# Kernel optimization log

Measured on AMD Instinct MI355X. Metric: run time of the kernel, lower is better.

Reference implementation:

```python
import jax, jax.numpy as jnp
import numpy as np

B, S, D_MODEL = 1, 2048, 2048
N_HEADS, N_KV_HEADS, D_HEAD = 16, 4, 128
ROTARY_DIM, ROTARY_BASE = 128, 10000.0
ATTN_SCALE = float(np.sqrt(D_HEAD))
REPEAT = N_HEADS // N_KV_HEADS


def _sin_cos_rotary(n_ctx, rotary_dim, base):
    # TransformerLens calculate_sin_cos_rotary, rotary_adjacent_pairs=False:
    # freq repeated as 'd -> (2 d)'
    pos = jnp.arange(n_ctx, dtype=jnp.float32)
    dim = jnp.arange(rotary_dim // 2, dtype=jnp.float32)
    freq = base ** (dim / (rotary_dim / 2))
    freq = jnp.concatenate([freq, freq])  # (2 d)
    angles = pos[:, None] / freq[None, :]  # [n_ctx, rotary_dim]
    return jnp.sin(angles), jnp.cos(angles)


def _rotate_every_two_half(x):
    # rotate_half for non-adjacent pairs: [-x2, x1]
    d = x.shape[-1]
    return jnp.concatenate([-x[..., d // 2:], x[..., : d // 2]], axis=-1)


def _apply_rotary(x, sin, cos):
    # x: [batch, pos, head, d_head]; sin/cos: [n_ctx, rotary_dim]
    p = x.shape[1]
    s = sin[:p][:, None, :]  # [pos, 1, rotary_dim]
    c = cos[:p][:, None, :]
    x_rot = x[..., :ROTARY_DIM]
    x_pass = x[..., ROTARY_DIM:]
    x_rotated = x_rot * c + _rotate_every_two_half(x_rot) * s
    return jnp.concatenate([x_rotated, x_pass], axis=-1)


def setup_inputs() -> dict:
    key = jax.random.key(0)
    ks = jax.random.split(key, 10)
    init = 1.0 / np.sqrt(D_MODEL)
    return {
        "query_input": jax.random.normal(ks[0], (B, S, D_MODEL), jnp.float32),
        "key_input": jax.random.normal(ks[1], (B, S, D_MODEL), jnp.float32),
        "value_input": jax.random.normal(ks[2], (B, S, D_MODEL), jnp.float32),
        "W_Q": jax.random.normal(ks[3], (N_HEADS, D_MODEL, D_HEAD), jnp.float32) * init,
        "b_Q": jnp.zeros((N_HEADS, D_HEAD), jnp.float32),
        "W_K": jax.random.normal(ks[4], (N_KV_HEADS, D_MODEL, D_HEAD), jnp.float32) * init,
        "b_K": jnp.zeros((N_KV_HEADS, D_HEAD), jnp.float32),
        "W_V": jax.random.normal(ks[5], (N_KV_HEADS, D_MODEL, D_HEAD), jnp.float32) * init,
        "b_V": jnp.zeros((N_KV_HEADS, D_HEAD), jnp.float32),
        "W_O": jax.random.normal(ks[6], (N_HEADS, D_HEAD, D_MODEL), jnp.float32) * init,
        "b_O": jnp.zeros((D_MODEL,), jnp.float32),
    }


def reference(query_input, key_input, value_input, W_Q, b_Q, W_K, b_K, W_V, b_V, W_O, b_O):
    sin, cos = _sin_cos_rotary(S, ROTARY_DIM, ROTARY_BASE)

    # Projections
    q = jnp.einsum("bpd,hdk->bphk", query_input, W_Q) + b_Q   # [B,S,H,dh]
    k = jnp.einsum("bpd,hdk->bphk", key_input, W_K) + b_K     # [B,S,Hkv,dh]
    v = jnp.einsum("bpd,hdk->bphk", value_input, W_V) + b_V   # [B,S,Hkv,dh]

    # Rotary on q and k (before KV head expansion)
    q = _apply_rotary(q, sin, cos)
    k = _apply_rotary(k, sin, cos)

    # GQA expansion via repeat_interleave on head dim
    k = jnp.repeat(k, REPEAT, axis=2)  # [B,S,H,dh]
    v = jnp.repeat(v, REPEAT, axis=2)

    # Attention scores, causal mask, softmax
    scores = jnp.einsum("bqhd,bkhd->bhqk", q, k) / ATTN_SCALE  # [B,H,S,S]
    causal = jnp.tril(jnp.ones((S, S), dtype=bool))
    scores = jnp.where(causal, scores, jnp.finfo(scores.dtype).min)
    pattern = jax.nn.softmax(scores, axis=-1)

    # Weighted values and output projection
    z = jnp.einsum("bhqk,bkhd->bqhd", pattern, v)              # [B,S,H,dh]
    out = jnp.einsum("bqhd,hdm->bqm", z, W_O) + b_O            # [B,S,D]
    return out
```

## Files before the change

### kernel.cpp

```cpp
#include <hip/hip_runtime.h>
#include <hip/hip_bf16.h>
#include <stdint.h>
#include <math.h>

typedef __bf16 bf16_t;
typedef __attribute__((ext_vector_type(8))) __bf16 bf16x8;
typedef __attribute__((ext_vector_type(4))) __bf16 bf16x4;
typedef __attribute__((ext_vector_type(4))) float f32x4;
typedef __attribute__((ext_vector_type(16))) float f32x16;
typedef unsigned int uint2v __attribute__((ext_vector_type(2)));

static constexpr int S = 2048;
static constexpr int DM = 2048;
static constexpr int NH = 16;
static constexpr int NKV = 4;
static constexpr int DH = 128;

#define MFMA16(a, b, c) __builtin_amdgcn_mfma_f32_16x16x32_bf16((a), (b), (c), 0, 0, 0)
#define MFMA32(a, b, c) __builtin_amdgcn_mfma_f32_32x32x16_bf16((a), (b), (c), 0, 0, 0)

__device__ __forceinline__ void gload_lds16(const void* g, void* l) {
  __builtin_amdgcn_global_load_lds((__attribute__((address_space(1))) void*)(g),
                                   (__attribute__((address_space(3))) void*)(l), 16, 0, 0);
}

template <int N>
__device__ __forceinline__ void wait_vmcnt() {
  asm volatile("s_waitcnt vmcnt(%0)" :: "n"(N) : "memory");
}
__device__ __forceinline__ void wait_lgkm0() {
  asm volatile("s_waitcnt lgkmcnt(0)" ::: "memory");
}

__device__ __forceinline__ unsigned cvtpk(float lo, float hi) {
  unsigned r;
  asm("v_cvt_pk_bf16_f32 %0, %1, %2" : "=v"(r) : "v"(lo), "v"(hi));
  return r;
}
__device__ __forceinline__ void plswap2(unsigned& a, unsigned& b) {
  uint2v r = __builtin_amdgcn_permlane32_swap(a, b, false, false);
  a = r[0]; b = r[1];
}
__device__ __forceinline__ float swapred_max(float x) {
  uint2v r = __builtin_amdgcn_permlane32_swap(__float_as_uint(x), __float_as_uint(x), false, false);
  return fmaxf(__uint_as_float(r[0]), __uint_as_float(r[1]));
}
__device__ __forceinline__ float swapred_sum(float x) {
  uint2v r = __builtin_amdgcn_permlane32_swap(__float_as_uint(x), __float_as_uint(x), false, false);
  return __uint_as_float(r[0]) + __uint_as_float(r[1]);
}
__device__ __forceinline__ bf16x8 packfrag(float a0, float a1, float a2, float a3,
                                           float a4, float a5, float a6, float a7) {
  unsigned w0 = cvtpk(a0, a1), w1 = cvtpk(a2, a3);
  unsigned w2 = cvtpk(a4, a5), w3 = cvtpk(a6, a7);
  plswap2(w0, w2); plswap2(w1, w3);
  union { unsigned u[4]; bf16x8 v; } u;
  u.u[0] = w0; u.u[1] = w1; u.u[2] = w2; u.u[3] = w3;
  return u.v;
}

__device__ const unsigned char attn_map[61] = {
  120,121,122,123,124,125,126, 112,113,114,115,116,117, 104,105,106,107,108,109,
  96,97,98,99,100,101, 88,89,90,91,92, 80,81,82,83,84, 72,73,74,75, 64,65,66,67,
  56,57,58,59, 48,49,50, 40,41,42, 32,33, 24,25, 16,17, 8, 0};
__device__ const unsigned char sbase[16] = {0,0,0,2,4,6,9,12,16,20,24,29,34,40,46,52};

__global__ __launch_bounds__(256)
void prep_k(const float* __restrict__ Xq, const float* __restrict__ Xk,
            const float* __restrict__ Xv, const float* __restrict__ WQ,
            const float* __restrict__ WK, const float* __restrict__ WV,
            const float* __restrict__ WO, float2* __restrict__ tab,
            bf16_t* __restrict__ xq, bf16_t* __restrict__ xk, bf16_t* __restrict__ xv,
            bf16_t* __restrict__ wqT, bf16_t* __restrict__ wkT, bf16_t* __restrict__ wvT,
            bf16_t* __restrict__ woT) {
  __shared__ float tile[32][33];
  const int b = blockIdx.x, t = threadIdx.x;
  if (b < 512) {
    int idx = b * 256 + t;
    int p = idx >> 6, j = idx & 63;
    double inv = exp2(-(double)j * 13.287712379549449 / 64.0);
    double ang = (double)p * inv;
    tab[idx] = make_float2((float)sin(ang), (float)cos(ang));
  } else if (b < 12800) {
    int i = ((b - 512) * 256 + t) * 4;
    const float* in; bf16_t* out; int off;
    if (i < 4194304) { in = Xq; out = xq; off = i; }
    else if (i < 8388608) { in = Xk; out = xk; off = i - 4194304; }
    else { in = Xv; out = xv; off = i - 8388608; }
    f32x4 v = *(const f32x4*)(in + off);
    bf16x4 o;
    o[0] = (bf16_t)v[0]; o[1] = (bf16_t)v[1]; o[2] = (bf16_t)v[2]; o[3] = (bf16_t)v[3];
    *(bf16x4*)(out + off) = o;
  } else if (b < 16896) {
    int b2 = b - 12800;
    int bx = b2 & 3, by = (b2 >> 2) & 63, bz = b2 >> 8;
    int c0 = bx * 32, r0 = by * 32;
    int tx = t & 31, ty = t >> 5;
    const float* src = WQ + (size_t)bz * 2048 * 128;
    #pragma unroll
    for (int j = 0; j < 32; j += 8)
      tile[ty + j][tx] = src[(size_t)(r0 + ty + j) * 128 + c0 + tx];
    __syncthreads();
    #pragma unroll
    for (int j = 0; j < 32; j += 8)
      wqT[(size_t)(bz * 128 + c0 + ty + j) * 2048 + r0 + tx] = (bf16_t)tile[tx][ty + j];
  } else if (b < 18944) {
    int b2 = b - 16896;
    int bx = b2 & 3, by = (b2 >> 2) & 63, bz = b2 >> 8;
    int g = bz & 3;
    const float* in = (bz < 4) ? WK : WV;
    bf16_t* out = (bz < 4) ? wkT : wvT;
    int c0 = bx * 32, r0 = by * 32;
    int tx = t & 31, ty = t >> 5;
    const float* src = in + (size_t)g * 2048 * 128;
    #pragma unroll
    for (int j = 0; j < 32; j += 8)
      tile[ty + j][tx] = src[(size_t)(r0 + ty + j) * 128 + c0 + tx];
    __syncthreads();
    #pragma unroll
    for (int j = 0; j < 32; j += 8)
      out[(size_t)(g * 128 + c0 + ty + j) * 2048 + r0 + tx] = (bf16_t)tile[tx][ty + j];
  } else {
    int b2 = b - 18944;
    int bx = b2 & 63, by = (b2 >> 6) & 3, bz = b2 >> 8;
    int c0 = bx * 32, r0 = by * 32;
    int tx = t & 31, ty = t >> 5;
    const float* src = WO + (size_t)bz * 128 * 2048;
    #pragma unroll
    for (int j = 0; j < 32; j += 8)
      tile[ty + j][tx] = src[(size_t)(r0 + ty + j) * 2048 + c0 + tx];
    __syncthreads();
    #pragma unroll
    for (int j = 0; j < 32; j += 8)
      woT[(size_t)(c0 + ty + j) * 2048 + bz * 128 + r0 + tx] = (bf16_t)tile[tx][ty + j];
  }
}

__global__ void rope_qk_k(bf16_t* __restrict__ Qb, bf16_t* __restrict__ Kb,
                          const float2* __restrict__ tab, float qscale) {
  int tid = blockIdx.x * 256 + threadIdx.x;
  int row = tid >> 4;
  int i = (tid & 15) * 4;
  bf16_t* base; float scale;
  if (row < NH * S) { base = Qb + (size_t)row * DH; scale = qscale; }
  else { base = Kb + (size_t)(row - NH * S) * DH; scale = 1.0f; }
  int p = row & (S - 1);
  bf16x4 lo = *(bf16x4*)(base + i);
  bf16x4 hi = *(bf16x4*)(base + i + 64);
  float4 t0 = *(const float4*)(tab + p * 64 + i);
  float4 t1 = *(const float4*)(tab + p * 64 + i + 2);
  float sv[4] = {t0.x, t0.z, t1.x, t1.z};
  float cv[4] = {t0.y, t0.w, t1.y, t1.w};
  bf16x4 nlo, nhi;
  #pragma unroll
  for (int j = 0; j < 4; ++j) {
    float a = (float)lo[j], b = (float)hi[j];
    nlo[j] = (bf16_t)((a * cv[j] - b * sv[j]) * scale);
    nhi[j] = (bf16_t)((b * cv[j] + a * sv[j]) * scale);
  }
  *(bf16x4*)(base + i) = nlo;
  *(bf16x4*)(base + i + 64) = nhi;
}

__global__ __launch_bounds__(256)
void proj_gemm_k(const bf16_t* __restrict__ xq, const bf16_t* __restrict__ xk,
                 const bf16_t* __restrict__ xv, const bf16_t* __restrict__ wqT,
                 const bf16_t* __restrict__ wkT, const bf16_t* __restrict__ wvT,
                 const float* __restrict__ bQ, const float* __restrict__ bK,
                 const float* __restrict__ bV, bf16_t* __restrict__ Qb,
                 bf16_t* __restrict__ Kb, bf16_t* __restrict__ Vt) {
  const int b = blockIdx.x;
  const int xcd = b & 7, idx = b >> 3;
  const int nb = (xcd & 3) * 12 + idx % 12;
  const int m0 = ((xcd >> 2) * 8 + idx / 12) * 128;
  const bf16_t* A; const bf16_t* B; const float* bias; bf16_t* dst; int ncol0;
  bool vmode = false;
  if (nb < 32)      { A = xq; B = wqT; bias = bQ; dst = Qb; ncol0 = nb * 64; }
  else if (nb < 40) { A = xk; B = wkT; bias = bK; dst = Kb; ncol0 = (nb - 32) * 64; }
  else              { A = xv; B = wvT; bias = bV; dst = Vt; ncol0 = (nb - 40) * 64; vmode = true; }
  const int K = 2048;
  const int t = threadIdx.x;
  const int lane = t & 63, w = t >> 6;
  const int l15 = lane & 15, lg = lane >> 4;
  const int wr = (w >> 1) * 64, wc = (w & 1) * 32;

  __shared__ bf16_t lA[2][128 * 64];
  __shared__ bf16_t lB[2][64 * 64];

  f32x4 acc[4][2] = {};
  const int srow = t >> 3;
  const int sslot = t & 7;

  auto stage = [&](int buf, int kt) {
    #pragma unroll
    for (int i = 0; i < 4; ++i) {
      int row = i * 32 + srow;
      int ss = sslot ^ (row & 7);
      gload_lds16(A + (size_t)(m0 + row) * K + kt * 64 + ss * 8,
                  (void*)(&lA[buf][0] + i * 2048 + t * 8));
    }
    #pragma unroll
    for (int i = 0; i < 2; ++i) {
      int row = i * 32 + srow;
      int ss = sslot ^ (row & 7);
      gload_lds16(B + (size_t)(ncol0 + row) * K + kt * 64 + ss * 8,
                  (void*)(&lB[buf][0] + i * 2048 + t * 8));
    }
  };

  const int nk = K >> 6;
  stage(0, 0);
  for (int kt = 0; kt < nk; ++kt) {
    const int cur = kt & 1;
    if (kt + 1 < nk) {
      stage(cur ^ 1, kt + 1);
      wait_vmcnt<6>();
    } else {
      wait_vmcnt<0>();
    }
    __builtin_amdgcn_s_barrier();
    #pragma unroll
    for (int kk = 0; kk < 2; ++kk) {
      bf16x8 af[4], bfv[2];
      #pragma unroll
      for (int f = 0; f < 4; ++f) {
        int row = wr + f * 16 + l15;
        int slot = kk * 4 + lg;
        af[f] = *(const bf16x8*)(&lA[cur][0] + row * 64 + ((slot ^ (row & 7)) * 8));
      }
      #pragma unroll
      for (int f = 0; f < 2; ++f) {
        int row = wc + f * 16 + l15;
        int slot = kk * 4 + lg;
        bfv[f] = *(const bf16x8*)(&lB[cur][0] + row * 64 + ((slot ^ (row & 7)) * 8));
      }
      #pragma unroll
      for (int fm = 0; fm < 4; ++fm)
        #pragma unroll
        for (int fn = 0; fn < 2; ++fn)
          acc[fm][fn] = MFMA16(af[fm], bfv[fn], acc[fm][fn]);
    }
    wait_lgkm0();
    __builtin_amdgcn_s_barrier();
  }

  #pragma unroll
  for (int fm = 0; fm < 4; ++fm) {
    int rowb = m0 + wr + fm * 16 + lg * 4;
    #pragma unroll
    for (int fn = 0; fn < 2; ++fn) {
      int col = ncol0 + wc + fn * 16 + l15;
      float bb = bias[col];
      if (vmode) {
        bf16x4 pk;
        #pragma unroll
        for (int r = 0; r < 4; ++r) pk[r] = (bf16_t)(acc[fm][fn][r] + bb);
        *(bf16x4*)(dst + (size_t)col * S + rowb) = pk;
      } else {
        #pragma unroll
        for (int r = 0; r < 4; ++r) {
          float v = acc[fm][fn][r] + bb;
          dst[((size_t)(col >> 7) * S + (rowb + r)) * DH + (col & 127)] = (bf16_t)v;
        }
      }
    }
  }
}

__global__ __launch_bounds__(256)
void gemm_o_k(const bf16_t* __restrict__ A, const bf16_t* __restrict__ B,
              const float* __restrict__ bias, float* __restrict__ Cout) {
  const int b = blockIdx.x;
  const int xcd = b & 7, idx = b >> 3;
  const int ncol0 = ((xcd & 3) * 8 + (idx & 7)) * 64;
  const int m0 = (((xcd >> 2) * 8) + (idx >> 3)) * 128;
  const int K = 2048;
  const int t = threadIdx.x;
  const int lane = t & 63, w = t >> 6;
  const int l15 = lane & 15, lg = lane >> 4;
  const int wr = (w >> 1) * 64, wc = (w & 1) * 32;

  __shared__ bf16_t lA[2][128 * 64];
  __shared__ bf16_t lB[2][64 * 64];

  f32x4 acc[4][2] = {};
  const int srow = t >> 3;
  const int sslot = t & 7;

  auto stage = [&](int buf, int kt) {
    #pragma unroll
    for (int i = 0; i < 4; ++i) {
      int row = i * 32 + srow;
      int ss = sslot ^ (row & 7);
      gload_lds16(A + (size_t)(m0 + row) * K + kt * 64 + ss * 8,
                  (void*)(&lA[buf][0] + i * 2048 + t * 8));
    }
    #pragma unroll
    for (int i = 0; i < 2; ++i) {
      int row = i * 32 + srow;
      int ss = sslot ^ (row & 7);
      gload_lds16(B + (size_t)(ncol0 + row) * K + kt * 64 + ss * 8,
                  (void*)(&lB[buf][0] + i * 2048 + t * 8));
    }
  };

  const int nk = K >> 6;
  stage(0, 0);
  for (int kt = 0; kt < nk; ++kt) {
    const int cur = kt & 1;
    if (kt + 1 < nk) {
      stage(cur ^ 1, kt + 1);
      wait_vmcnt<6>();
    } else {
      wait_vmcnt<0>();
    }
    __builtin_amdgcn_s_barrier();
    #pragma unroll
    for (int kk = 0; kk < 2; ++kk) {
      bf16x8 af[4], bfv[2];
      #pragma unroll
      for (int f = 0; f < 4; ++f) {
        int row = wr + f * 16 + l15;
        int slot = kk * 4 + lg;
        af[f] = *(const bf16x8*)(&lA[cur][0] + row * 64 + ((slot ^ (row & 7)) * 8));
      }
      #pragma unroll
      for (int f = 0; f < 2; ++f) {
        int row = wc + f * 16 + l15;
        int slot = kk * 4 + lg;
        bfv[f] = *(const bf16x8*)(&lB[cur][0] + row * 64 + ((slot ^ (row & 7)) * 8));
      }
      #pragma unroll
      for (int fm = 0; fm < 4; ++fm)
        #pragma unroll
        for (int fn = 0; fn < 2; ++fn)
          acc[fm][fn] = MFMA16(af[fm], bfv[fn], acc[fm][fn]);
    }
    wait_lgkm0();
    __builtin_amdgcn_s_barrier();
  }

  #pragma unroll
  for (int fm = 0; fm < 4; ++fm) {
    int rowb = m0 + wr + fm * 16 + lg * 4;
    #pragma unroll
    for (int fn = 0; fn < 2; ++fn) {
      int col = ncol0 + wc + fn * 16 + l15;
      float bb = bias[col];
      #pragma unroll
      for (int r = 0; r < 4; ++r)
        Cout[(size_t)(rowb + r) * DM + col] = acc[fm][fn][r] + bb;
    }
  }
}

__global__ __launch_bounds__(256, 2)
void attn_k(const bf16_t* __restrict__ Q, const bf16_t* __restrict__ K,
            const bf16_t* __restrict__ Vt, bf16_t* __restrict__ Z,
            bf16_t* __restrict__ Opart, float* __restrict__ mpart,
            float* __restrict__ lpart) {
  const int bid = blockIdx.x;
  const int h = bid & 15;
  const int g = bid >> 4;
  const int code = attn_map[g];
  const int qb = code >> 3, ci = code & 7;
  const bool split = qb >= 2;
  const int kt0 = 5 * ci;
  const int kteA = 5 * ci + 4, kteB = 2 * qb + 1;
  const int ktend = kteA < kteB ? kteA : kteB;
  const int q0 = qb * 128;
  const int hkv = h >> 2;
  const int t = threadIdx.x;
  const int lane = t & 63, w = t >> 6;
  const int l31 = lane & 31, hi = lane >> 5;
  const int qrow = q0 + w * 32 + l31;

  __shared__ bf16_t lK[2][64 * 128];
  __shared__ bf16_t lV[2][128 * 64];

  bf16x8 qf[8];
  #pragma unroll
  for (int j = 0; j < 8; ++j)
    qf[j] = *(const bf16x8*)(Q + ((size_t)h * S + qrow) * DH + j * 16 + hi * 8);

  auto stageKV = [&](int buf, int kt) {
    #pragma unroll
    for (int i = 0; i < 4; ++i) {
      int row = i * 16 + (t >> 4);
      int ss = (t & 15) ^ (row & 15);
      gload_lds16(K + ((size_t)hkv * S + kt * 64 + row) * DH + ss * 8,
                  (void*)(&lK[buf][0] + i * 2048 + t * 8));
    }
    #pragma unroll
    for (int i = 0; i < 4; ++i) {
      int row = i * 32 + (t >> 3);
      int ss = (t & 7) ^ (row & 7);
      gload_lds16(Vt + ((size_t)hkv * DH + row) * S + kt * 64 + ss * 8,
                  (void*)(&lV[buf][0] + i * 2048 + t * 8));
    }
  };

  f32x16 oacc0 = {}, oacc1 = {}, oacc2 = {}, oacc3 = {};
  float m_run = -3.0e3f, l_run = 0.f;

  stageKV(0, kt0);
  for (int kt = kt0; kt <= ktend; ++kt) {
    const int cur = (kt - kt0) & 1;
    if (kt < ktend) {
      stageKV(cur ^ 1, kt + 1);
      wait_vmcnt<8>();
    } else {
      wait_vmcnt<0>();
    }
    __builtin_amdgcn_s_barrier();

    f32x16 s0 = {}, s1 = {};
    __builtin_amdgcn_s_setprio(1);
    #pragma unroll
    for (int j = 0; j < 8; ++j) {
      int sIdx = j * 2 + hi;
      int r0 = l31;
      bf16x8 k0 = *(const bf16x8*)(&lK[cur][0] + r0 * 128 + ((sIdx ^ (r0 & 15)) * 8));
      s0 = MFMA32(k0, qf[j], s0);
      int r1 = 32 + l31;
      bf16x8 k1 = *(const bf16x8*)(&lK[cur][0] + r1 * 128 + ((sIdx ^ (r1 & 15)) * 8));
      s1 = MFMA32(k1, qf[j], s1);
    }
    __builtin_amdgcn_s_setprio(0);

    if (kt >= 2 * qb) {
      #pragma unroll
      for (int r = 0; r < 16; ++r) {
        int krow = kt * 64 + (r & 3) + 8 * (r >> 2) + 4 * hi;
        if (krow > qrow) s0[r] = -1e30f;
        if (krow + 32 > qrow) s1[r] = -1e30f;
      }
    }

    float mxa = s0[0], mxb = s0[1], mxc = s0[2], mxd = s0[3];
    #pragma unroll
    for (int r = 4; r < 16; r += 4) {
      mxa = fmaxf(mxa, s0[r]); mxb = fmaxf(mxb, s0[r + 1]);
      mxc = fmaxf(mxc, s0[r + 2]); mxd = fmaxf(mxd, s0[r + 3]);
    }
    #pragma unroll
    for (int r = 0; r < 16; r += 4) {
      mxa = fmaxf(mxa, s1[r]); mxb = fmaxf(mxb, s1[r + 1]);
      mxc = fmaxf(mxc, s1[r + 2]); mxd = fmaxf(mxd, s1[r + 3]);
    }
    float mfull = swapred_max(fmaxf(fmaxf(mxa, mxb), fmaxf(mxc, mxd)));

    float m_new, alpha;
    bool nore = __all(mfull - m_run <= 8.0f);
    if (nore) { m_new = m_run; alpha = 1.0f; }
    else { m_new = fmaxf(m_run, mfull); alpha = exp2f(m_run - m_new); }

    float psa = 0.f, psb = 0.f, psc = 0.f, psd = 0.f;
    #pragma unroll
    for (int r = 0; r < 16; r += 4) {
      s0[r] = exp2f(s0[r] - m_new); psa += s0[r];
      s0[r + 1] = exp2f(s0[r + 1] - m_new); psb += s0[r + 1];
      s0[r + 2] = exp2f(s0[r + 2] - m_new); psc += s0[r + 2];
      s0[r + 3] = exp2f(s0[r + 3] - m_new); psd += s0[r + 3];
    }
    #pragma unroll
    for (int r = 0; r < 16; r += 4) {
      s1[r] = exp2f(s1[r] - m_new); psa += s1[r];
      s1[r + 1] = exp2f(s1[r + 1] - m_new); psb += s1[r + 1];
      s1[r + 2] = exp2f(s1[r + 2] - m_new); psc += s1[r + 2];
      s1[r + 3] = exp2f(s1[r + 3] - m_new); psd += s1[r + 3];
    }
    float lt = swapred_sum((psa + psb) + (psc + psd));
    l_run = l_run * alpha + lt;
    m_run = m_new;

    if (!nore) {
      #pragma unroll
      for (int r = 0; r < 16; ++r) {
        int qs = (r & 3) + 8 * (r >> 2) + 4 * hi;
        float ar = __shfl(alpha, qs);
        oacc0[r] *= ar; oacc1[r] *= ar; oacc2[r] *= ar; oacc3[r] *= ar;
      }
    }

    bf16x8 pa[4];
    pa[0] = packfrag(s0[0], s0[1], s0[2], s0[3], s0[4], s0[5], s0[6], s0[7]);
    pa[1] = packfrag(s0[8], s0[9], s0[10], s0[11], s0[12], s0[13], s0[14], s0[15]);
    pa[2] = packfrag(s1[0], s1[1], s1[2], s1[3], s1[4], s1[5], s1[6], s1[7]);
    pa[3] = packfrag(s1[8], s1[9], s1[10], s1[11], s1[12], s1[13], s1[14], s1[15]);

    __builtin_amdgcn_s_setprio(1);
#define PVBLK(OA, db) { \
    int dr = (db) * 32 + l31; \
    _Pragma("unroll") \
    for (int ks = 0; ks < 4; ++ks) { \
      int sIdx = ks * 2 + hi; \
      bf16x8 vf = *(const bf16x8*)(&lV[cur][0] + dr * 64 + ((sIdx ^ (dr & 7)) * 8)); \
      OA = MFMA32(pa[ks], vf, OA); \
    } }
    PVBLK(oacc0, 0)
    PVBLK(oacc1, 1)
    PVBLK(oacc2, 2)
    PVBLK(oacc3, 3)
#undef PVBLK
    __builtin_amdgcn_s_setprio(0);
    wait_lgkm0();
    __builtin_amdgcn_s_barrier();
  }

  if (!split) {
    float linv = 1.0f / l_run;
    #pragma unroll
    for (int r = 0; r < 16; ++r) {
      int qs = (r & 3) + 8 * (r >> 2) + 4 * hi;
      float lv = __shfl(linv, qs);
      int qg = q0 + w * 32 + qs;
      bf16_t* zp = Z + (size_t)qg * DM + h * DH + l31;
      zp[0]  = (bf16_t)(oacc0[r] * lv);
      zp[32] = (bf16_t)(oacc1[r] * lv);
      zp[64] = (bf16_t)(oacc2[r] * lv);
      zp[96] = (bf16_t)(oacc3[r] * lv);
    }
  } else {
    const int slot = h * 59 + sbase[qb] + ci;
    bf16_t* Op = Opart + (size_t)slot * 16384;
    #pragma unroll
    for (int r = 0; r < 16; ++r) {
      int qs = (r & 3) + 8 * (r >> 2) + 4 * hi;
      bf16_t* op = Op + (w * 32 + qs) * 128 + l31;
      op[0]  = (bf16_t)oacc0[r];
      op[32] = (bf16_t)oacc1[r];
      op[64] = (bf16_t)oacc2[r];
      op[96] = (bf16_t)oacc3[r];
    }
    if (lane < 32) {
      mpart[slot * 128 + w * 32 + l31] = m_run;
      lpart[slot * 128 + w * 32 + l31] = l_run;
    }
  }
}

__global__ void combine_k(const bf16_t* __restrict__ Opart, const float* __restrict__ mpart,
                          const float* __restrict__ lpart, bf16_t* __restrict__ Z) {
  int tid = blockIdx.x * 256 + threadIdx.x;
  int d4 = tid & 31;
  int q = (tid >> 5) & 127;
  int u = tid >> 12;
  int h = u / 14;
  int qb = 2 + (u - h * 14);
  int nc = (2 * qb + 6) / 5;
  int slot0 = h * 59 + sbase[qb];
  float M = -3.0e3f;
  for (int c = 0; c < nc; ++c) M = fmaxf(M, mpart[(slot0 + c) * 128 + q]);
  float L = 0.f;
  float o0 = 0.f, o1 = 0.f, o2 = 0.f, o3 = 0.f;
  for (int c = 0; c < nc; ++c) {
    float a = exp2f(mpart[(slot0 + c) * 128 + q] - M);
    L += a * lpart[(slot0 + c) * 128 + q];
    bf16x4 ov = *(const bf16x4*)(Opart + (size_t)(slot0 + c) * 16384 + q * 128 + d4 * 4);
    o0 += a * (float)ov[0]; o1 += a * (float)ov[1];
    o2 += a * (float)ov[2]; o3 += a * (float)ov[3];
  }
  float inv = 1.0f / L;
  bf16x4 zv;
  zv[0] = (bf16_t)(o0 * inv); zv[1] = (bf16_t)(o1 * inv);
  zv[2] = (bf16_t)(o2 * inv); zv[3] = (bf16_t)(o3 * inv);
  int qg = qb * 128 + q;
  *(bf16x4*)(Z + (size_t)qg * DM + h * DH + d4 * 4) = zv;
}

extern "C" void kernel_launch(void* const* d_in, const int* in_sizes, int n_in,
                              void* d_out, int out_size, void* d_ws, size_t ws_size,
                              hipStream_t stream) {
  (void)in_sizes; (void)n_in; (void)out_size; (void)ws_size;
  const float* Xq = (const float*)d_in[0];
  const float* Xk = (const float*)d_in[1];
  const float* Xv = (const float*)d_in[2];
  const float* WQ = (const float*)d_in[3];
  const float* bQ = (const float*)d_in[4];
  const float* WK = (const float*)d_in[5];
  const float* bK = (const float*)d_in[6];
  const float* WV = (const float*)d_in[7];
  const float* bV = (const float*)d_in[8];
  const float* WO = (const float*)d_in[9];
  const float* bO = (const float*)d_in[10];

  char* w = (char*)d_ws;
  float2* tab = (float2*)w;
  bf16_t* xq  = (bf16_t*)(w + (1 << 20));
  bf16_t* xk  = xq + 4194304;
  bf16_t* xv  = xk + 4194304;
  bf16_t* wqT = xv + 4194304;
  bf16_t* wkT = wqT + 4194304;
  bf16_t* wvT = wkT + 1048576;
  bf16_t* woT = wvT + 1048576;
  bf16_t* Qb  = woT + 4194304;
  bf16_t* Kb  = Qb + 4194304;
  bf16_t* Vtb = Kb + 1048576;
  bf16_t* Zb  = Vtb + 1048576;
  bf16_t* Opart = xq;
  float* mpart = (float*)tab;
  float* lpart = mpart + 944 * 128;

  prep_k<<<dim3(23040), dim3(256), 0, stream>>>(Xq, Xk, Xv, WQ, WK, WV, WO, tab,
                                                xq, xk, xv, wqT, wkT, wvT, woT);

  proj_gemm_k<<<dim3(768), dim3(256), 0, stream>>>(xq, xk, xv, wqT, wkT, wvT,
                                                   bQ, bK, bV, Qb, Kb, Vtb);

  const float qscale = 1.4426950408889634f / sqrtf(128.0f);
  rope_qk_k<<<dim3(2560), dim3(256), 0, stream>>>(Qb, Kb, tab, qscale);

  attn_k<<<dim3(976), dim3(256), 0, stream>>>(Qb, Kb, Vtb, Zb, Opart, mpart, lpart);
  combine_k<<<dim3(3584), dim3(256), 0, stream>>>(Opart, mpart, lpart, Zb);

  gemm_o_k<<<dim3(512), dim3(256), 0, stream>>>(Zb, woT, bO, (float*)d_out);
}
```

Baseline: 142.8 us.

## Use 128-key attention tiles with single-buffered K/V and resplit work chunks

```diff
diff --git a/kernel.cpp b/kernel.cpp
--- a/kernel.cpp
+++ b/kernel.cpp
@@ -59,11 +59,11 @@
   return u.v;
 }
 
-__device__ const unsigned char attn_map[61] = {
-  120,121,122,123,124,125,126, 112,113,114,115,116,117, 104,105,106,107,108,109,
-  96,97,98,99,100,101, 88,89,90,91,92, 80,81,82,83,84, 72,73,74,75, 64,65,66,67,
-  56,57,58,59, 48,49,50, 40,41,42, 32,33, 24,25, 16,17, 8, 0};
-__device__ const unsigned char sbase[16] = {0,0,0,2,4,6,9,12,16,20,24,29,34,40,46,52};
+__device__ const unsigned char attn_map[51] = {
+  120,121,122,123,124, 112,113,114,115,116, 104,105,106,107, 96,97,98,99,
+  88,89,90,91, 80,81,82, 72,73,74, 64,65,66, 56,57, 48,49, 40,41, 32, 24, 16,
+  108, 83, 58, 33, 8, 125, 100, 75, 50, 25, 0};
+__device__ const unsigned char sbase[16] = {0,0,0,0,2,4,6,9,12,15,19,23,27,32,37,42};
 
 __global__ __launch_bounds__(256)
 void prep_k(const float* __restrict__ Xq, const float* __restrict__ Xk,
@@ -364,10 +364,9 @@
   const int g = bid >> 4;
   const int code = attn_map[g];
   const int qb = code >> 3, ci = code & 7;
-  const bool split = qb >= 2;
-  const int kt0 = 5 * ci;
-  const int kteA = 5 * ci + 4, kteB = 2 * qb + 1;
-  const int ktend = kteA < kteB ? kteA : kteB;
+  const bool split = qb >= 3;
+  const int it0 = 3 * ci;
+  const int itend = (3 * ci + 2 < qb) ? (3 * ci + 2) : qb;
   const int q0 = qb * 128;
   const int hkv = h >> 2;
   const int t = threadIdx.x;
@@ -375,78 +374,75 @@
   const int l31 = lane & 31, hi = lane >> 5;
   const int qrow = q0 + w * 32 + l31;
 
-  __shared__ bf16_t lK[2][64 * 128];
-  __shared__ bf16_t lV[2][128 * 64];
+  __shared__ bf16_t lK[128 * 128];
+  __shared__ bf16_t lV[128 * 128];
 
   bf16x8 qf[8];
   #pragma unroll
   for (int j = 0; j < 8; ++j)
     qf[j] = *(const bf16x8*)(Q + ((size_t)h * S + qrow) * DH + j * 16 + hi * 8);
 
-  auto stageKV = [&](int buf, int kt) {
-    #pragma unroll
-    for (int i = 0; i < 4; ++i) {
+  auto stageKV = [&](int it) {
+    #pragma unroll
+    for (int i = 0; i < 8; ++i) {
       int row = i * 16 + (t >> 4);
       int ss = (t & 15) ^ (row & 15);
-      gload_lds16(K + ((size_t)hkv * S + kt * 64 + row) * DH + ss * 8,
-                  (void*)(&lK[buf][0] + i * 2048 + t * 8));
-    }
-    #pragma unroll
-    for (int i = 0; i < 4; ++i) {
-      int row = i * 32 + (t >> 3);
-      int ss = (t & 7) ^ (row & 7);
-      gload_lds16(Vt + ((size_t)hkv * DH + row) * S + kt * 64 + ss * 8,
-                  (void*)(&lV[buf][0] + i * 2048 + t * 8));
+      gload_lds16(K + ((size_t)hkv * S + it * 128 + row) * DH + ss * 8,
+                  (void*)(lK + i * 2048 + t * 8));
+    }
+    #pragma unroll
+    for (int i = 0; i < 8; ++i) {
+      int row = i * 16 + (t >> 4);
+      int ss = (t & 15) ^ (row & 15);
+      gload_lds16(Vt + ((size_t)hkv * DH + row) * S + it * 128 + ss * 8,
+                  (void*)(lV + i * 2048 + t * 8));
     }
   };
 
   f32x16 oacc0 = {}, oacc1 = {}, oacc2 = {}, oacc3 = {};
   float m_run = -3.0e3f, l_run = 0.f;
-
-  stageKV(0, kt0);
-  for (int kt = kt0; kt <= ktend; ++kt) {
-    const int cur = (kt - kt0) & 1;
-    if (kt < ktend) {
-      stageKV(cur ^ 1, kt + 1);
-      wait_vmcnt<8>();
-    } else {
-      wait_vmcnt<0>();
-    }
+  const int msk = l31 & 15;
+
+  for (int it = it0; it <= itend; ++it) {
     __builtin_amdgcn_s_barrier();
-
-    f32x16 s0 = {}, s1 = {};
+    stageKV(it);
+    wait_vmcnt<8>();
+    __builtin_amdgcn_s_barrier();
+
+    f32x16 s0 = {}, s1 = {}, s2 = {}, s3 = {};
     __builtin_amdgcn_s_setprio(1);
-    #pragma unroll
-    for (int j = 0; j < 8; ++j) {
-      int sIdx = j * 2 + hi;
-      int r0 = l31;
-      bf16x8 k0 = *(const bf16x8*)(&lK[cur][0] + r0 * 128 + ((sIdx ^ (r0 & 15)) * 8));
-      s0 = MFMA32(k0, qf[j], s0);
-      int r1 = 32 + l31;
-      bf16x8 k1 = *(const bf16x8*)(&lK[cur][0] + r1 * 128 + ((sIdx ^ (r1 & 15)) * 8));
-      s1 = MFMA32(k1, qf[j], s1);
-    }
+#define QKG(SN, N) { \
+    const bf16_t* rb = lK + ((N) * 32 + l31) * 128; \
+    _Pragma("unroll") \
+    for (int j = 0; j < 8; ++j) { \
+      bf16x8 kf = *(const bf16x8*)(rb + (((j * 2 + hi) ^ msk) * 8)); \
+      SN = MFMA32(kf, qf[j], SN); \
+    } }
+    QKG(s0, 0) QKG(s1, 1) QKG(s2, 2) QKG(s3, 3)
+#undef QKG
     __builtin_amdgcn_s_setprio(0);
 
-    if (kt >= 2 * qb) {
-      #pragma unroll
-      for (int r = 0; r < 16; ++r) {
-        int krow = kt * 64 + (r & 3) + 8 * (r >> 2) + 4 * hi;
-        if (krow > qrow) s0[r] = -1e30f;
-        if (krow + 32 > qrow) s1[r] = -1e30f;
-      }
-    }
-
-    float mxa = s0[0], mxb = s0[1], mxc = s0[2], mxd = s0[3];
+    if (it == qb) {
+#define MASKG(SN, N) { \
+      _Pragma("unroll") \
+      for (int r = 0; r < 16; ++r) { \
+        int key = it * 128 + (N) * 32 + (r & 3) + 8 * (r >> 2) + 4 * hi; \
+        if (key > qrow) SN[r] = -1e30f; \
+      } }
+      MASKG(s0, 0) MASKG(s1, 1) MASKG(s2, 2) MASKG(s3, 3)
+#undef MASKG
+    }
+
+    float mxa = fmaxf(fmaxf(s0[0], s1[0]), fmaxf(s2[0], s3[0]));
+    float mxb = fmaxf(fmaxf(s0[1], s1[1]), fmaxf(s2[1], s3[1]));
+    float mxc = fmaxf(fmaxf(s0[2], s1[2]), fmaxf(s2[2], s3[2]));
+    float mxd = fmaxf(fmaxf(s0[3], s1[3]), fmaxf(s2[3], s3[3]));
     #pragma unroll
     for (int r = 4; r < 16; r += 4) {
-      mxa = fmaxf(mxa, s0[r]); mxb = fmaxf(mxb, s0[r + 1]);
-      mxc = fmaxf(mxc, s0[r + 2]); mxd = fmaxf(mxd, s0[r + 3]);
-    }
-    #pragma unroll
-    for (int r = 0; r < 16; r += 4) {
-      mxa = fmaxf(mxa, s1[r]); mxb = fmaxf(mxb, s1[r + 1]);
-      mxc = fmaxf(mxc, s1[r + 2]); mxd = fmaxf(mxd, s1[r + 3]);
+      mxa = fmaxf(mxa, fmaxf(fmaxf(s0[r], s1[r]), fmaxf(s2[r], s3[r])));
+      mxb = fmaxf(mxb, fmaxf(fmaxf(s0[r+1], s1[r+1]), fmaxf(s2[r+1], s3[r+1])));
+      mxc = fmaxf(mxc, fmaxf(fmaxf(s0[r+2], s1[r+2]), fmaxf(s2[r+2], s3[r+2])));
+      mxd = fmaxf(mxd, fmaxf(fmaxf(s0[r+3], s1[r+3]), fmaxf(s2[r+3], s3[r+3])));
     }
     float mfull = swapred_max(fmaxf(fmaxf(mxa, mxb), fmaxf(mxc, mxd)));
 
@@ -456,20 +452,16 @@
     else { m_new = fmaxf(m_run, mfull); alpha = exp2f(m_run - m_new); }
 
     float psa = 0.f, psb = 0.f, psc = 0.f, psd = 0.f;
-    #pragma unroll
-    for (int r = 0; r < 16; r += 4) {
-      s0[r] = exp2f(s0[r] - m_new); psa += s0[r];
-      s0[r + 1] = exp2f(s0[r + 1] - m_new); psb += s0[r + 1];
-      s0[r + 2] = exp2f(s0[r + 2] - m_new); psc += s0[r + 2];
-      s0[r + 3] = exp2f(s0[r + 3] - m_new); psd += s0[r + 3];
-    }
-    #pragma unroll
-    for (int r = 0; r < 16; r += 4) {
-      s1[r] = exp2f(s1[r] - m_new); psa += s1[r];
-      s1[r + 1] = exp2f(s1[r + 1] - m_new); psb += s1[r + 1];
-      s1[r + 2] = exp2f(s1[r + 2] - m_new); psc += s1[r + 2];
-      s1[r + 3] = exp2f(s1[r + 3] - m_new); psd += s1[r + 3];
-    }
+#define EXPG(SN) { \
+    _Pragma("unroll") \
+    for (int r = 0; r < 16; r += 4) { \
+      SN[r] = exp2f(SN[r] - m_new); psa += SN[r]; \
+      SN[r+1] = exp2f(SN[r+1] - m_new); psb += SN[r+1]; \
+      SN[r+2] = exp2f(SN[r+2] - m_new); psc += SN[r+2]; \
+      SN[r+3] = exp2f(SN[r+3] - m_new); psd += SN[r+3]; \
+    } }
+    EXPG(s0) EXPG(s1) EXPG(s2) EXPG(s3)
+#undef EXPG
     float lt = swapred_sum((psa + psb) + (psc + psd));
     l_run = l_run * alpha + lt;
     m_run = m_new;
@@ -483,29 +475,31 @@
       }
     }
 
-    bf16x8 pa[4];
+    bf16x8 pa[8];
     pa[0] = packfrag(s0[0], s0[1], s0[2], s0[3], s0[4], s0[5], s0[6], s0[7]);
     pa[1] = packfrag(s0[8], s0[9], s0[10], s0[11], s0[12], s0[13], s0[14], s0[15]);
     pa[2] = packfrag(s1[0], s1[1], s1[2], s1[3], s1[4], s1[5], s1[6], s1[7]);
     pa[3] = packfrag(s1[8], s1[9], s1[10], s1[11], s1[12], s1[13], s1[14], s1[15]);
+    pa[4] = packfrag(s2[0], s2[1], s2[2], s2[3], s2[4], s2[5], s2[6], s2[7]);
+    pa[5] = packfrag(s2[8], s2[9], s2[10], s2[11], s2[12], s2[13], s2[14], s2[15]);
+    pa[6] = packfrag(s3[0], s3[1], s3[2], s3[3], s3[4], s3[5], s3[6], s3[7]);
+    pa[7] = packfrag(s3[8], s3[9], s3[10], s3[11], s3[12], s3[13], s3[14], s3[15]);
+
+    wait_vmcnt<0>();
+    __builtin_amdgcn_s_barrier();
 
     __builtin_amdgcn_s_setprio(1);
-#define PVBLK(OA, db) { \
-    int dr = (db) * 32 + l31; \
+#define PVG(OA, DB) { \
+    const bf16_t* vb = lV + ((DB) * 32 + l31) * 128; \
     _Pragma("unroll") \
-    for (int ks = 0; ks < 4; ++ks) { \
-      int sIdx = ks * 2 + hi; \
-      bf16x8 vf = *(const bf16x8*)(&lV[cur][0] + dr * 64 + ((sIdx ^ (dr & 7)) * 8)); \
+    for (int ks = 0; ks < 8; ++ks) { \
+      bf16x8 vf = *(const bf16x8*)(vb + (((ks * 2 + hi) ^ msk) * 8)); \
       OA = MFMA32(pa[ks], vf, OA); \
     } }
-    PVBLK(oacc0, 0)
-    PVBLK(oacc1, 1)
-    PVBLK(oacc2, 2)
-    PVBLK(oacc3, 3)
-#undef PVBLK
+    PVG(oacc0, 0) PVG(oacc1, 1) PVG(oacc2, 2) PVG(oacc3, 3)
+#undef PVG
     __builtin_amdgcn_s_setprio(0);
     wait_lgkm0();
-    __builtin_amdgcn_s_barrier();
   }
 
   if (!split) {
@@ -522,7 +516,7 @@
       zp[96] = (bf16_t)(oacc3[r] * lv);
     }
   } else {
-    const int slot = h * 59 + sbase[qb] + ci;
+    const int slot = h * 48 + sbase[qb] + ci;
     bf16_t* Op = Opart + (size_t)slot * 16384;
     #pragma unroll
     for (int r = 0; r < 16; ++r) {
@@ -546,10 +540,10 @@
   int d4 = tid & 31;
   int q = (tid >> 5) & 127;
   int u = tid >> 12;
-  int h = u / 14;
-  int qb = 2 + (u - h * 14);
-  int nc = (2 * qb + 6) / 5;
-  int slot0 = h * 59 + sbase[qb];
+  int h = u / 13;
+  int qb = 3 + (u - h * 13);
+  int nc = (qb + 3) / 3;
+  int slot0 = h * 48 + sbase[qb];
   float M = -3.0e3f;
   for (int c = 0; c < nc; ++c) M = fmaxf(M, mpart[(slot0 + c) * 128 + q]);
   float L = 0.f;
@@ -600,7 +594,7 @@
   bf16_t* Zb  = Vtb + 1048576;
   bf16_t* Opart = xq;
   float* mpart = (float*)tab;
-  float* lpart = mpart + 944 * 128;
+  float* lpart = mpart + 768 * 128;
 
   prep_k<<<dim3(23040), dim3(256), 0, stream>>>(Xq, Xk, Xv, WQ, WK, WV, WO, tab,
                                                 xq, xk, xv, wqT, wkT, wvT, woT);
@@ -611,8 +605,8 @@
   const float qscale = 1.4426950408889634f / sqrtf(128.0f);
   rope_qk_k<<<dim3(2560), dim3(256), 0, stream>>>(Qb, Kb, tab, qscale);
 
-  attn_k<<<dim3(976), dim3(256), 0, stream>>>(Qb, Kb, Vtb, Zb, Opart, mpart, lpart);
-  combine_k<<<dim3(3584), dim3(256), 0, stream>>>(Opart, mpart, lpart, Zb);
+  attn_k<<<dim3(816), dim3(256), 0, stream>>>(Qb, Kb, Vtb, Zb, Opart, mpart, lpart);
+  combine_k<<<dim3(3328), dim3(256), 0, stream>>>(Opart, mpart, lpart, Zb);
 
   gemm_o_k<<<dim3(512), dim3(256), 0, stream>>>(Zb, woT, bO, (float*)d_out);
 }
```

Measured after the change: 138.4 us. 1.03x faster.
